# Optimization experiments

Measured on AMD Instinct MI355X. Metric: run time of the kernel, lower is better.

The kernel has to match this reference:

```python
import jax, jax.numpy as jnp
import numpy as np

NUM_NODES = 50000
NUM_FEATS = 64
NUM_HEADS = 2
NUM_EDGES = 800000


def setup_inputs() -> dict:
    key = jax.random.key(0)
    k1, k2, k3 = jax.random.split(key, 3)
    x = jax.random.normal(k1, (NUM_NODES, NUM_FEATS), dtype=jnp.float32)
    # qk_lin: Linear(num_feats, 2*num_feats*num_heads)
    lim = 1.0 / np.sqrt(NUM_FEATS)
    W_qk = jax.random.uniform(k2, (NUM_FEATS, 2 * NUM_HEADS * NUM_FEATS),
                              dtype=jnp.float32, minval=-lim, maxval=lim)
    b_qk = jnp.zeros((2 * NUM_HEADS * NUM_FEATS,), dtype=jnp.float32)
    edge_index = jax.random.randint(k3, (2, NUM_EDGES), 0, NUM_NODES, dtype=jnp.int32)
    return {"x": x, "W_qk": W_qk, "b_qk": b_qk, "edge_index": edge_index}


def reference(x, W_qk, b_qk, edge_index):
    """Edge-restricted multi-head QK attention with sparse softmax over
    each row's outgoing edges, averaged over heads. Returns per-edge
    attention values [E] (sparse COO values; indices == edge_index)."""
    N, F = x.shape
    H = W_qk.shape[1] // (2 * F)
    # qk: [N, 2*H*F] -> [N, H, 2, F]; q/k split matches einops rearranges
    qk = (x @ W_qk + b_qk).reshape(N, H, 2, F)
    q = qk[:, :, 0, :]  # [N, H, F]
    k = qk[:, :, 1, :]  # [N, H, F]
    row, col = edge_index[0], edge_index[1]
    # per-edge per-head scores: q[row] . k[col]  -> [E, H]
    s = jnp.einsum('ehf,ehf->eh', q[row], k[col])
    # sparse softmax over dim=2 (columns) == segment softmax grouped by row
    m = jax.ops.segment_max(s, row, num_segments=N)      # [N, H]
    ex = jnp.exp(s - m[row])                             # [E, H]
    denom = jax.ops.segment_sum(ex, row, num_segments=N)  # [N, H]
    p = ex / denom[row]                                  # [E, H]
    # torch.sparse.sum over heads / num_heads == mean over heads
    return jnp.mean(p, axis=1)  # [E]
```

## Files before the change

kernel.cpp:

```cpp
#include <hip/hip_runtime.h>
#include <hip/hip_bf16.h>


#define NFEAT 64
#define NCOL  256
#define WT_STRIDE 72

typedef __attribute__((ext_vector_type(8))) short bf16x8;
typedef __attribute__((ext_vector_type(4))) float f32x4;
typedef __attribute__((ext_vector_type(4))) unsigned int u32x4;

__device__ __forceinline__ unsigned short f2bf(float f) {
    union { __hip_bfloat16 h; unsigned short u; } cv;
    cv.h = __float2bfloat16(f);
    return cv.u;
}

__device__ __forceinline__ float dot_bf16x2(unsigned a, unsigned b) {
    float alo = __uint_as_float(a << 16), ahi = __uint_as_float(a & 0xFFFF0000u);
    float blo = __uint_as_float(b << 16), bhi = __uint_as_float(b & 0xFFFF0000u);
    return alo * blo + ahi * bhi;
}

__global__ __launch_bounds__(256) void gemm_qk_mfma(
    const float* __restrict__ x, const float* __restrict__ W,
    const float* __restrict__ b,
    unsigned short* __restrict__ qo, unsigned short* __restrict__ ko,
    float* __restrict__ den, int N)
{
    __shared__ unsigned short WtL[NCOL * WT_STRIDE];
    __shared__ float bL[NCOL];
    const int tid = threadIdx.x;

    for (int i = tid; i < NFEAT * NCOL; i += 256) {
        const int kk = i >> 8, c = i & 255;
        WtL[c * WT_STRIDE + kk] = f2bf(W[i]);
    }
    bL[tid] = b[tid];

    const int t = blockIdx.x * 256 + tid;
    if (t < 2 * N) den[t] = 0.f;

    const int lane = tid & 63;
    const int wv   = tid >> 6;
    const int l15  = lane & 15;
    const int quad = lane >> 4;
    const int base = blockIdx.x * 128 + wv * 32;
    __syncthreads();

    if (base >= N) return;

    bf16x8 afrag[2][2];
#pragma unroll
    for (int s = 0; s < 2; ++s) {
        int m = base + s * 16 + l15;
        if (m >= N) m = N - 1;
        const float* xp = x + (size_t)m * NFEAT + quad * 8;
#pragma unroll
        for (int ks = 0; ks < 2; ++ks) {
            float4 a0 = *(const float4*)(xp + ks * 32);
            float4 a1 = *(const float4*)(xp + ks * 32 + 4);
            bf16x8 f;
            f[0] = f2bf(a0.x); f[1] = f2bf(a0.y); f[2] = f2bf(a0.z); f[3] = f2bf(a0.w);
            f[4] = f2bf(a1.x); f[5] = f2bf(a1.y); f[6] = f2bf(a1.z); f[7] = f2bf(a1.w);
            afrag[s][ks] = f;
        }
    }

#pragma unroll 4
    for (int ct = 0; ct < 16; ++ct) {
        const int c = ct * 16 + l15;
        bf16x8 b0 = *(const bf16x8*)(WtL + (size_t)c * WT_STRIDE + quad * 8);
        bf16x8 b1 = *(const bf16x8*)(WtL + (size_t)c * WT_STRIDE + 32 + quad * 8);
        const float bias = bL[c];
        const int h   = c >> 7;
        const int isk = (c >> 6) & 1;
        const int f0  = c & 63;
        unsigned short* dst = isk ? ko : qo;
#pragma unroll
        for (int s = 0; s < 2; ++s) {
            f32x4 acc = {0.f, 0.f, 0.f, 0.f};
            acc = __builtin_amdgcn_mfma_f32_16x16x32_bf16(afrag[s][0], b0, acc, 0, 0, 0);
            acc = __builtin_amdgcn_mfma_f32_16x16x32_bf16(afrag[s][1], b1, acc, 0, 0, 0);
#pragma unroll
            for (int r = 0; r < 4; ++r) {
                const int m = base + s * 16 + quad * 4 + r;
                if (m < N)
                    dst[(size_t)m * 128 + h * 64 + f0] = f2bf(acc[r] + bias);
            }
        }
    }
}

__global__ __launch_bounds__(256) void edge_scores_exp(
    const unsigned short* __restrict__ q, const unsigned short* __restrict__ k,
    const int* __restrict__ ei, float* __restrict__ ex_out,
    float* __restrict__ denom, int E)
{
    const int grp  = (int)((blockIdx.x * 256 + threadIdx.x) >> 4);
    const int lane = threadIdx.x & 15;
    const int g0   = grp * 4;
    if (g0 >= E) return;

    int v = 0;
    if (lane < 4)      v = ei[g0 + lane];
    else if (lane < 8) v = ei[E + g0 + (lane - 4)];
    int rows[4], cols[4];
#pragma unroll
    for (int i = 0; i < 4; ++i) {
        rows[i] = __shfl(v, i, 16);
        cols[i] = __shfl(v, 4 + i, 16);
    }

    u32x4 qa[4], ka[4];
#pragma unroll
    for (int i = 0; i < 4; ++i) {
        qa[i] = ((const u32x4*)(q + (size_t)rows[i] * 128))[lane];
        ka[i] = ((const u32x4*)(k + (size_t)cols[i] * 128))[lane];
    }
    asm volatile("" :: "v"(qa[0]), "v"(qa[1]), "v"(qa[2]), "v"(qa[3]),
                       "v"(ka[0]), "v"(ka[1]), "v"(ka[2]), "v"(ka[3]));

#pragma unroll
    for (int i = 0; i < 4; ++i) {
        float p = dot_bf16x2(qa[i][0], ka[i][0]) + dot_bf16x2(qa[i][1], ka[i][1])
                + dot_bf16x2(qa[i][2], ka[i][2]) + dot_bf16x2(qa[i][3], ka[i][3]);
        p += __shfl_xor(p, 1);
        p += __shfl_xor(p, 2);
        p += __shfl_xor(p, 4);
        if ((lane & 7) == 0 && g0 + i < E) {
            const int h  = lane >> 3;
            const float e = __expf(p);
            ex_out[(size_t)(g0 + i) * 2 + h] = e;
            __hip_atomic_fetch_add(&denom[(size_t)rows[i] * 2 + h], e,
                                   __ATOMIC_RELAXED, __HIP_MEMORY_SCOPE_AGENT);
        }
    }
}

__global__ __launch_bounds__(256) void edge_out_k(
    const int* __restrict__ ei, const float* __restrict__ ex,
    const float* __restrict__ denom, float* __restrict__ out, int E)
{
    const int e = blockIdx.x * 256 + threadIdx.x;
    if (e >= E) return;
    const int row = ei[e];
    const float2 exv = *(const float2*)&ex[(size_t)e * 2];
    const float2 dv  = *(const float2*)&denom[(size_t)row * 2];
    out[e] = 0.5f * (exv.x / dv.x + exv.y / dv.y);
}

extern "C" void kernel_launch(void* const* d_in, const int* in_sizes, int n_in,
                              void* d_out, int out_size, void* d_ws, size_t ws_size,
                              hipStream_t stream)
{
    const float* x   = (const float*)d_in[0];
    const float* W   = (const float*)d_in[1];
    const float* b   = (const float*)d_in[2];
    const int*   ei  = (const int*)d_in[3];
    float*       out = (float*)d_out;

    const int N = in_sizes[0] / NFEAT;
    const int E = in_sizes[3] / 2;

    char* ws = (char*)d_ws;
    size_t off = 0;
    auto alloc = [&](size_t bytes) { void* p = ws + off; off += (bytes + 255) & ~(size_t)255; return p; };
    unsigned short* q_ws  = (unsigned short*)alloc((size_t)N * 128 * 2);
    unsigned short* k_ws  = (unsigned short*)alloc((size_t)N * 128 * 2);
    float*          ex_ws = (float*)alloc((size_t)E * 2 * sizeof(float));
    float*          den_ws= (float*)alloc((size_t)N * 2 * sizeof(float));
    (void)ws_size;

    gemm_qk_mfma<<<(N + 127) / 128, 256, 0, stream>>>(x, W, b, q_ws, k_ws, den_ws, N);
    edge_scores_exp<<<((size_t)(E + 3) / 4 * 16 + 255) / 256, 256, 0, stream>>>(q_ws, k_ws, ei, ex_ws, den_ws, E);
    edge_out_k<<<(E + 255) / 256, 256, 0, stream>>>(ei, ex_ws, den_ws, out, E);
}
```

Before: 141.2 us.

## Transpose MFMA operands in QK GEMM to emit vectorized packed bf16 stores

The QK projection GEMM now feeds the weights as the MFMA A operand and the x rows as the B operand, so each lane's accumulator holds four consecutive output columns of one node. Those four values get the bias added from a single float4 LDS read and are written as one 8-byte packed bf16 store, replacing four scattered 2-byte stores. Each wave now handles 16 rows instead of 32, so the grid doubles. That means every block repeats the full weight conversion into LDS, which adds global reads and conversion work to the GEMM.

```diff
diff --git a/kernel.cpp b/kernel.cpp
--- a/kernel.cpp
+++ b/kernel.cpp
@@ -9,6 +9,7 @@
 typedef __attribute__((ext_vector_type(8))) short bf16x8;
 typedef __attribute__((ext_vector_type(4))) float f32x4;
 typedef __attribute__((ext_vector_type(4))) unsigned int u32x4;
+typedef __attribute__((ext_vector_type(4))) unsigned short u16x4;
 
 __device__ __forceinline__ unsigned short f2bf(float f) {
     union { __hip_bfloat16 h; unsigned short u; } cv;
@@ -45,50 +46,50 @@
     const int wv   = tid >> 6;
     const int l15  = lane & 15;
     const int quad = lane >> 4;
-    const int base = blockIdx.x * 128 + wv * 32;
+    const int base = blockIdx.x * 64 + wv * 16;
     __syncthreads();
 
     if (base >= N) return;
 
-    bf16x8 afrag[2][2];
+    int m = base + l15;
+    if (m >= N) m = N - 1;
+    const float* xp = x + (size_t)m * NFEAT + quad * 8;
+    bf16x8 xf[2];
 #pragma unroll
-    for (int s = 0; s < 2; ++s) {
-        int m = base + s * 16 + l15;
-        if (m >= N) m = N - 1;
-        const float* xp = x + (size_t)m * NFEAT + quad * 8;
-#pragma unroll
-        for (int ks = 0; ks < 2; ++ks) {
-            float4 a0 = *(const float4*)(xp + ks * 32);
-            float4 a1 = *(const float4*)(xp + ks * 32 + 4);
-            bf16x8 f;
-            f[0] = f2bf(a0.x); f[1] = f2bf(a0.y); f[2] = f2bf(a0.z); f[3] = f2bf(a0.w);
-            f[4] = f2bf(a1.x); f[5] = f2bf(a1.y); f[6] = f2bf(a1.z); f[7] = f2bf(a1.w);
-            afrag[s][ks] = f;
-        }
+    for (int ks = 0; ks < 2; ++ks) {
+        float4 a0 = *(const float4*)(xp + ks * 32);
+        float4 a1 = *(const float4*)(xp + ks * 32 + 4);
+        bf16x8 f;
+        f[0] = f2bf(a0.x); f[1] = f2bf(a0.y); f[2] = f2bf(a0.z); f[3] = f2bf(a0.w);
+        f[4] = f2bf(a1.x); f[5] = f2bf(a1.y); f[6] = f2bf(a1.z); f[7] = f2bf(a1.w);
+        xf[ks] = f;
     }
+
+    const int mst = base + l15;
+    const bool mok = (mst < N);
 
 #pragma unroll 4
     for (int ct = 0; ct < 16; ++ct) {
         const int c = ct * 16 + l15;
-        bf16x8 b0 = *(const bf16x8*)(WtL + (size_t)c * WT_STRIDE + quad * 8);
-        bf16x8 b1 = *(const bf16x8*)(WtL + (size_t)c * WT_STRIDE + 32 + quad * 8);
-        const float bias = bL[c];
-        const int h   = c >> 7;
-        const int isk = (c >> 6) & 1;
-        const int f0  = c & 63;
-        unsigned short* dst = isk ? ko : qo;
-#pragma unroll
-        for (int s = 0; s < 2; ++s) {
-            f32x4 acc = {0.f, 0.f, 0.f, 0.f};
-            acc = __builtin_amdgcn_mfma_f32_16x16x32_bf16(afrag[s][0], b0, acc, 0, 0, 0);
-            acc = __builtin_amdgcn_mfma_f32_16x16x32_bf16(afrag[s][1], b1, acc, 0, 0, 0);
-#pragma unroll
-            for (int r = 0; r < 4; ++r) {
-                const int m = base + s * 16 + quad * 4 + r;
-                if (m < N)
-                    dst[(size_t)m * 128 + h * 64 + f0] = f2bf(acc[r] + bias);
-            }
-        }
+        bf16x8 wt0 = *(const bf16x8*)(WtL + (size_t)c * WT_STRIDE + quad * 8);
+        bf16x8 wt1 = *(const bf16x8*)(WtL + (size_t)c * WT_STRIDE + 32 + quad * 8);
+
+        f32x4 acc = {0.f, 0.f, 0.f, 0.f};
+        acc = __builtin_amdgcn_mfma_f32_16x16x32_bf16(wt0, xf[0], acc, 0, 0, 0);
+        acc = __builtin_amdgcn_mfma_f32_16x16x32_bf16(wt1, xf[1], acc, 0, 0, 0);
+
+        const int c0 = ct * 16 + quad * 4;
+        const float4 b4 = *(const float4*)&bL[c0];
+        u16x4 pk;
+        pk[0] = f2bf(acc[0] + b4.x);
+        pk[1] = f2bf(acc[1] + b4.y);
+        pk[2] = f2bf(acc[2] + b4.z);
+        pk[3] = f2bf(acc[3] + b4.w);
+        const int h  = c0 >> 7;
+        const int f0 = c0 & 63;
+        unsigned short* dst = ((c0 >> 6) & 1) ? ko : qo;
+        if (mok)
+            *(u16x4*)(dst + (size_t)mst * 128 + h * 64 + f0) = pk;
     }
 }
 
@@ -172,7 +173,7 @@
     float*          den_ws= (float*)alloc((size_t)N * 2 * sizeof(float));
     (void)ws_size;
 
-    gemm_qk_mfma<<<(N + 127) / 128, 256, 0, stream>>>(x, W, b, q_ws, k_ws, den_ws, N);
+    gemm_qk_mfma<<<(N + 63) / 64, 256, 0, stream>>>(x, W, b, q_ws, k_ws, den_ws, N);
     edge_scores_exp<<<((size_t)(E + 3) / 4 * 16 + 255) / 256, 256, 0, stream>>>(q_ws, k_ws, ei, ex_ws, den_ws, E);
     edge_out_k<<<(E + 255) / 256, 256, 0, stream>>>(ei, ex_ws, den_ws, out, E);
 }
```

After: 142.4 us (median of 2 runs). No clear change (+0.8%).
